# Performance work log

Hardware: AMD Instinct MI355X
Metric: run time of the kernel (lower is better)

Reference implementation:

```python
import jax, jax.numpy as jnp
import numpy as np

B, CIN, COUT, RES, WDIM, K, GN_GROUPS = 8, 512, 512, 64, 512, 3, 32


def setup_inputs() -> dict:
    key = jax.random.key(0)
    ks = jax.random.split(key, 6)
    return dict(
        x=jax.random.normal(ks[0], (B, CIN, RES, RES), jnp.float32),
        w=jax.random.normal(ks[1], (B, WDIM), jnp.float32),
        noise=jax.random.normal(ks[2], (B, 1, RES, RES), jnp.float32),
        weight=jax.random.normal(ks[3], (COUT, CIN, K, K), jnp.float32),
        bias=jnp.zeros((COUT,), jnp.float32),
        affine_W=jax.random.normal(ks[4], (3 * CIN, WDIM), jnp.float32),
        affine_b=jnp.ones((3 * CIN,), jnp.float32),  # bias_init=1
        gn_weight=jnp.ones((CIN,), jnp.float32),
        gn_bias=jnp.zeros((CIN,), jnp.float32),
        gamma=jnp.full((1, COUT, 1, 1), 1e-5, jnp.float32),  # layer_scale_init
        noise_strength=jnp.asarray(0.1, jnp.float32),
    )


def _group_norm_f32(x, weight, bias, groups=GN_GROUPS, eps=1e-5):
    # GroupNorm_float32: normalize in float32, cast back to x.dtype
    b, c, h, w = x.shape
    xf = x.astype(jnp.float32).reshape(b, groups, c // groups, h, w)
    mu = xf.mean(axis=(2, 3, 4), keepdims=True)
    var = xf.var(axis=(2, 3, 4), keepdims=True)
    xn = ((xf - mu) * jax.lax.rsqrt(var + eps)).reshape(b, c, h, w)
    return (xn * weight[None, :, None, None] + bias[None, :, None, None]).astype(x.dtype)


def reference(x, w, noise, weight, bias, affine_W, affine_b, gn_weight, gn_bias, gamma, noise_strength):
    b, cin, h, wd = x.shape
    cout, _, kh, kw = weight.shape
    # StyleSplit: FullyConnectedLayer (weight scaled by 1/sqrt(in_features)) then m1*m2+m3
    s = w @ (affine_W.T / jnp.sqrt(jnp.float32(w.shape[1]))) + affine_b  # [B, 3*Cin]
    m1, m2, m3 = jnp.split(s, 3, axis=1)
    styles = m1 * m2 + m3  # [B, Cin]
    # residual path: GroupNorm (float32) first
    xn = _group_norm_f32(x, gn_weight, gn_bias)
    # modulated_conv2d (fused path): per-sample modulate + demodulate
    wmod = weight[None] * styles[:, None, :, None, None]                 # [B,Cout,Cin,K,K]
    dcoef = jax.lax.rsqrt(jnp.sum(jnp.square(wmod), axis=(2, 3, 4)) + 1e-8)  # [B,Cout]
    wmod = wmod * dcoef[:, :, None, None, None]
    # grouped conv with groups = batch (StyleGAN batch-as-groups trick)
    xg = xn.reshape(1, b * cin, h, wd)
    wg = wmod.reshape(b * cout, cin, kh, kw)
    pad = kh // 2
    y = jax.lax.conv_general_dilated(
        xg, wg, window_strides=(1, 1), padding=[(pad, pad), (pad, pad)],
        dimension_numbers=('NCHW', 'OIHW', 'NCHW'), feature_group_count=b)
    y = y.reshape(b, cout, h, wd)
    # noise injection
    y = y + noise * noise_strength
    # fused bias + lrelu with gain = bias_def_gain['lrelu'] * gain = sqrt(2) * 2
    act_gain = np.sqrt(2.0) * 2.0
    y = jax.nn.leaky_relu(y + bias[None, :, None, None], 0.2) * act_gain
    # layer-scale + residual (residual uses the normalized x) * sqrt(2)
    y = (gamma * y + xn) * np.sqrt(2.0)
    return y
```

## Files before the change

### kernel.cpp

```cpp
#include <hip/hip_runtime.h>
#include <hip/hip_bf16.h>

typedef short short8 __attribute__((ext_vector_type(8)));
typedef float f32x4 __attribute__((ext_vector_type(4)));

#define SWZ(c) (((c) & 3) ^ (((c) >> 2) & 3))
#define UNROLL _Pragma("unroll")

static __device__ __forceinline__ unsigned short f2bf(float f) {
    union { float f; unsigned u; } v; v.f = f;
    unsigned r = v.u + 0x7FFFu + ((v.u >> 16) & 1u);
    return (unsigned short)(r >> 16);
}

static __device__ __forceinline__ void gload16(const void* g, void* l) {
    __builtin_amdgcn_global_load_lds(
        (const __attribute__((address_space(1))) unsigned int*)g,
        (__attribute__((address_space(3))) unsigned int*)l, 16, 0, 0);
}

__global__ __launch_bounds__(256) void prep1(
    const float* __restrict__ x, const float* __restrict__ w,
    const float* __restrict__ affW, const float* __restrict__ affb,
    const float* __restrict__ weight,
    float* __restrict__ styles, float* __restrict__ meanv,
    float* __restrict__ rstdv, unsigned short* __restrict__ wpk,
    unsigned short* __restrict__ zp)
{
    __shared__ float ld[9 * 128];
    __shared__ float rs[4], rq[4];
    const int bid = blockIdx.x, t = threadIdx.x;

    if (bid < 256) {
        const float4* p = (const float4*)(x + (size_t)bid * 65536);
        float s = 0.f, q = 0.f;
#pragma unroll 4
        for (int k = 0; k < 64; ++k) {
            float4 v = p[t + (k << 8)];
            s += v.x + v.y + v.z + v.w;
            q += v.x * v.x + v.y * v.y + v.z * v.z + v.w * v.w;
        }
        for (int off = 32; off; off >>= 1) { s += __shfl_xor(s, off); q += __shfl_xor(q, off); }
        if ((t & 63) == 0) { rs[t >> 6] = s; rq[t >> 6] = q; }
        __syncthreads();
        if (t == 0) {
            float S = rs[0] + rs[1] + rs[2] + rs[3];
            float Q = rq[0] + rq[1] + rq[2] + rq[3];
            float mu = S * (1.f / 65536.f);
            float var = Q * (1.f / 65536.f) - mu * mu;
            meanv[bid] = mu;
            rstdv[bid] = rsqrtf(var + 1e-5f);
        }
    } else if (bid < 512) {
        int idx = bid - 256, bx = idx & 31, b = idx >> 5;
        int lane = t & 63, wv = t >> 6;
        float wr[8];
        const float* wb = w + b * 512 + lane * 8;
        UNROLL for (int r = 0; r < 8; ++r) wr[r] = wb[r];
        for (int ii = 0; ii < 4; ++ii) {
            int i = bx * 16 + wv * 4 + ii;
            float d[3];
            UNROLL for (int jj = 0; jj < 3; ++jj) {
                const float* a = affW + (size_t)(jj * 512 + i) * 512 + lane * 8;
                float dd = 0.f;
                UNROLL for (int r = 0; r < 8; ++r) dd += wr[r] * a[r];
                for (int off = 32; off; off >>= 1) dd += __shfl_xor(dd, off);
                d[jj] = dd;
            }
            if (lane == 0) {
                const float inv = 0.044194173824159216f;
                float s0 = d[0] * inv + affb[i];
                float s1 = d[1] * inv + affb[512 + i];
                float s2 = d[2] * inv + affb[1024 + i];
                styles[b * 512 + i] = s0 * s1 + s2;
            }
        }
    } else if (bid < 2560) {
        int idx = bid - 512, co = idx >> 2, c4 = idx & 3;
        const float* src = weight + (size_t)co * 4608 + c4 * 1152;
        for (int f = t; f < 1152; f += 256)
            ld[(f % 9) * 128 + (f / 9)] = src[f];
        __syncthreads();
        unsigned short* dst = wpk + (size_t)co * 4608 + c4 * 128;
        for (int f = t; f < 1152; f += 256) {
            int tap = f >> 7, ci = f & 127;
            dst[tap * 512 + ci] = f2bf(ld[tap * 128 + ci]);
        }
    } else {
        *(short8*)&zp[t * 8] = (short8)0;
    }
}

__global__ __launch_bounds__(256) void prep2(
    const float* __restrict__ x, const float* __restrict__ weight,
    const float* __restrict__ styles, const float* __restrict__ gnw,
    const float* __restrict__ gnb, const float* __restrict__ meanv,
    const float* __restrict__ rstdv,
    float* __restrict__ dcoef, unsigned short* __restrict__ xm)
{
    __shared__ float st2[8 * 512];
    __shared__ float red[32];
    __shared__ float sA[512], sB[512];
    __shared__ unsigned short tr[32 * 520];
    const int bid = blockIdx.x, t = threadIdx.x;

    if (bid < 512) {
        int co = bid;
        for (int i = t; i < 4096; i += 256) { float s = styles[i]; st2[i] = s * s; }
        __syncthreads();
        float p[8] = {0, 0, 0, 0, 0, 0, 0, 0};
        UNROLL for (int half = 0; half < 2; ++half) {
            int ci = t * 2 + half;
            const float* wp = weight + ((size_t)co * 512 + ci) * 9;
            float wsq = 0.f;
            UNROLL for (int k = 0; k < 9; ++k) wsq += wp[k] * wp[k];
            UNROLL for (int b = 0; b < 8; ++b) p[b] += wsq * st2[b * 512 + ci];
        }
        int lane = t & 63, wv = t >> 6;
        UNROLL for (int b = 0; b < 8; ++b) {
            float v = p[b];
            for (int off = 32; off; off >>= 1) v += __shfl_xor(v, off);
            if (lane == 0) red[wv * 8 + b] = v;
        }
        __syncthreads();
        if (t < 8) {
            float s = red[t] + red[8 + t] + red[16 + t] + red[24 + t];
            dcoef[t * 512 + co] = rsqrtf(s + 1e-8f);
        }
    } else {
        int idx = bid - 512, b = idx >> 7, px0 = (idx & 127) * 32;
        for (int i = t; i < 512; i += 256) {
            int g = i >> 4;
            float mu = meanv[b * 32 + g], r = rstdv[b * 32 + g];
            float st = styles[b * 512 + i];
            float a = r * gnw[i];
            sA[i] = a * st;
            sB[i] = (gnb[i] - mu * a) * st;
        }
        __syncthreads();
        int p = t & 31, cb = t >> 5;
        const float* xb = x + (size_t)b * 512 * 4096 + px0 + p;
#pragma unroll 4
        for (int it = 0; it < 64; ++it) {
            int ci = cb + (it << 3);
            float v = xb[(size_t)ci * 4096];
            tr[p * 520 + ci] = f2bf(v * sA[ci] + sB[ci]);
        }
        __syncthreads();
        int gran = t & 63;
        UNROLL for (int k = 0; k < 8; ++k) {
            int pl = k * 4 + (t >> 6);
            short8 v = *(const short8*)&tr[pl * 520 + gran * 8];
            *(short8*)&xm[((size_t)(b * 4096 + px0 + pl) << 9) + gran * 8] = v;
        }
    }
}

#define STAGE_W(SLOT, CC_, DY_)                                                 \
    { char* wd_ = wlds + (SLOT) * 24576; int wadd_ = (DY_) * 1536 + (CC_) * 32; \
      UNROLL for (int q = 0; q < 3; ++q)                                        \
          gload16(wsrc_fix[q] + wadd_, wd_ + wdst_off[q]); }

#define STAGE_I(CC_)                                                            \
    { char* id_ = ilds + ((CC_) & 1) * 42240; int iadd_ = (CC_) * 32;           \
      UNROLL for (int q = 0; q < 5; ++q)                                        \
          gload16(isrc_fix[q] + iadd_, id_ + idst_off[q]); }

#define PHASE(DY, CCSEL, VMN, STAGES_)                                          \
  {                                                                             \
    char* wbase = wlds + (DY) * 24576;                                          \
    char* ibase = ilds + (CCSEL) * 42240 + (2 * wn + (DY)) * 4224;              \
    short8 a0[4], b0[8], a1[4], b1[8], a2[4], b2[8];                            \
    UNROLL for (int m = 0; m < 4; ++m)                                          \
        a0[m] = *(const short8*)(wbase + aoff[m]);                              \
    UNROLL for (int n = 0; n < 8; ++n)                                          \
        b0[n] = *(const short8*)(ibase + (n >> 2) * 4224 + boff[0][n & 3]);     \
    STAGES_                                                                     \
    asm volatile("s_barrier" ::: "memory");                                     \
    UNROLL for (int m = 0; m < 4; ++m)                                          \
        a1[m] = *(const short8*)(wbase + 8192 + aoff[m]);                       \
    UNROLL for (int n = 0; n < 8; ++n)                                          \
        b1[n] = *(const short8*)(ibase + (n >> 2) * 4224 + boff[1][n & 3]);     \
    __builtin_amdgcn_s_setprio(1);                                              \
    UNROLL for (int m = 0; m < 4; ++m)                                          \
        UNROLL for (int n = 0; n < 8; ++n)                                      \
            acc[m][n] = __builtin_amdgcn_mfma_f32_16x16x32_bf16(                \
                a0[m], b0[n], acc[m][n], 0, 0, 0);                              \
    UNROLL for (int m = 0; m < 4; ++m)                                          \
        a2[m] = *(const short8*)(wbase + 16384 + aoff[m]);                      \
    UNROLL for (int n = 0; n < 8; ++n)                                          \
        b2[n] = *(const short8*)(ibase + (n >> 2) * 4224 + boff[2][n & 3]);     \
    UNROLL for (int m = 0; m < 4; ++m)                                          \
        UNROLL for (int n = 0; n < 8; ++n)                                      \
            acc[m][n] = __builtin_amdgcn_mfma_f32_16x16x32_bf16(                \
                a1[m], b1[n], acc[m][n], 0, 0, 0);                              \
    UNROLL for (int m = 0; m < 4; ++m)                                          \
        UNROLL for (int n = 0; n < 8; ++n)                                      \
            acc[m][n] = __builtin_amdgcn_mfma_f32_16x16x32_bf16(                \
                a2[m], b2[n], acc[m][n], 0, 0, 0);                              \
    __builtin_amdgcn_s_setprio(0);                                              \
    asm volatile("s_waitcnt vmcnt(" #VMN ")" ::: "memory");                     \
    asm volatile("s_barrier" ::: "memory");                                     \
  }

__global__ __launch_bounds__(512, 2) void conv3(
    const unsigned short* __restrict__ xm, const unsigned short* __restrict__ wpk,
    const unsigned short* __restrict__ zp,
    const float* __restrict__ x, const float* __restrict__ noise,
    const float* __restrict__ bias, const float* __restrict__ gnw,
    const float* __restrict__ gnb, const float* __restrict__ gamma,
    const float* __restrict__ dcoef, const float* __restrict__ meanv,
    const float* __restrict__ rstdv, const float* __restrict__ nsp,
    float* __restrict__ out)
{
    extern __shared__ char smem[];
    char* wlds = smem;
    char* ilds = smem + 73728;

    const int tid = threadIdx.x, lane = tid & 63, wv = tid >> 6;
    const int ct = blockIdx.x, pt = blockIdx.y, b = blockIdx.z;
    const int co0 = ct * 128, h0 = pt * 8;
    const int wm = wv >> 2, wn = wv & 3;
    const int lm = lane & 15, lg = lane >> 4;

    if (tid < 160) {
        int sel = tid / 80, rem = tid % 80;
        int r = rem >> 3, col = ((rem >> 2) & 1) * 65, g = rem & 3;
        *(short8*)(ilds + sel * 42240 + r * 4224 + col * 64 + g * 16) = (short8)0;
    }

    const unsigned short* wsrc_fix[3]; int wdst_off[3];
    UNROLL for (int q = 0; q < 3; ++q) {
        int k = q * 8 + wv;
        int id = k * 64 + lane;
        int dxid = id >> 9, co = (id >> 2) & 127, g = (id & 3) ^ SWZ(co);
        wsrc_fix[q] = wpk + (size_t)(co0 + co) * 4608 + dxid * 512 + g * 8;
        wdst_off[q] = k * 1024;
    }
    const unsigned short* isrc_fix[5]; int idst_off[5];
    UNROLL for (int q = 0; q < 5; ++q) {
        int k = q * 8 + wv;
        int r = k >> 2, chunk = k & 3;
        int idx = chunk * 64 + lane;
        int cimg = idx >> 2, gs = (idx & 3) ^ SWZ(cimg + 1);
        int imgrow = h0 - 1 + r;
        isrc_fix[q] = ((unsigned)imgrow < 64u)
            ? xm + (((size_t)(b * 4096 + imgrow * 64 + cimg)) << 9) + gs * 8
            : zp;
        idst_off[q] = r * 4224 + 64 + chunk * 1024;
    }

    int aoff[4];
    UNROLL for (int m = 0; m < 4; ++m) {
        int col = wm * 64 + m * 16 + lm;
        aoff[m] = col * 64 + (lg ^ SWZ(col)) * 16;
    }
    int boff[3][4];
    UNROLL for (int dx = 0; dx < 3; ++dx)
        UNROLL for (int nc = 0; nc < 4; ++nc) {
            int c = nc * 16 + lm + dx;
            boff[dx][nc] = c * 64 + (lg ^ SWZ(c)) * 16;
        }

    f32x4 acc[4][8];
    UNROLL for (int m = 0; m < 4; ++m)
        UNROLL for (int n = 0; n < 8; ++n) acc[m][n] = (f32x4){0.f, 0.f, 0.f, 0.f};

    STAGE_W(0, 0, 0)
    STAGE_I(0)
    STAGE_W(1, 0, 1)
    asm volatile("s_waitcnt lgkmcnt(0)" ::: "memory");
    asm volatile("s_waitcnt vmcnt(3)" ::: "memory");
    asm volatile("s_barrier" ::: "memory");

#pragma unroll 1
    for (int cc = 0; cc < 15; ++cc) {
        const int cs = cc & 1;
        PHASE(0, cs, 8, STAGE_W(2, cc, 2) STAGE_I(cc + 1))
        PHASE(1, cs, 8, STAGE_W(0, cc + 1, 0))
        PHASE(2, cs, 3, STAGE_W(1, cc + 1, 1))
    }
    PHASE(0, 1, 3, STAGE_W(2, 15, 2))
    PHASE(1, 1, 0, {})
    PHASE(2, 1, 0, {})

    const float nsv = *nsp;
    UNROLL for (int m = 0; m < 4; ++m) {
        UNROLL for (int n = 0; n < 8; ++n) {
            int pix = (h0 + 2 * wn + (n >> 2)) * 64 + (n & 3) * 16 + lm;
            float nz = noise[b * 4096 + pix] * nsv;
            UNROLL for (int j = 0; j < 4; ++j) {
                int co = co0 + wm * 64 + m * 16 + lg * 4 + j;
                int gidx = co >> 4;
                float v = acc[m][n][j] * dcoef[b * 512 + co] + nz + bias[co];
                float act = (v > 0.f ? v : 0.2f * v) * 2.8284271247461903f;
                float xv = x[((size_t)(b * 512 + co)) * 4096 + pix];
                float xn = (xv - meanv[b * 32 + gidx]) * rstdv[b * 32 + gidx] * gnw[co] + gnb[co];
                out[((size_t)(b * 512 + co)) * 4096 + pix] =
                    (gamma[co] * act + xn) * 1.4142135623730951f;
            }
        }
    }
}

extern "C" void kernel_launch(void* const* d_in, const int* in_sizes, int n_in,
                              void* d_out, int out_size, void* d_ws, size_t ws_size,
                              hipStream_t stream) {
    const float* x      = (const float*)d_in[0];
    const float* w      = (const float*)d_in[1];
    const float* noise  = (const float*)d_in[2];
    const float* weight = (const float*)d_in[3];
    const float* bias   = (const float*)d_in[4];
    const float* affW   = (const float*)d_in[5];
    const float* affb   = (const float*)d_in[6];
    const float* gnw    = (const float*)d_in[7];
    const float* gnb    = (const float*)d_in[8];
    const float* gamma  = (const float*)d_in[9];
    const float* nsp    = (const float*)d_in[10];
    float* out = (float*)d_out;

    char* ws = (char*)d_ws;
    float* styles = (float*)(ws + 0);
    float* dcoef  = (float*)(ws + 16384);
    float* meanv  = (float*)(ws + 32768);
    float* rstdv  = (float*)(ws + 33792);
    unsigned short* zp  = (unsigned short*)(ws + 34816);
    unsigned short* wpk = (unsigned short*)(ws + 38912);
    unsigned short* xm  = (unsigned short*)(ws + 4757504);

    hipFuncSetAttribute(reinterpret_cast<const void*>(conv3),
                        hipFuncAttributeMaxDynamicSharedMemorySize, 158208);

    prep1<<<dim3(2561), 256, 0, stream>>>(x, w, affW, affb, weight,
                                          styles, meanv, rstdv, wpk, zp);
    prep2<<<dim3(1536), 256, 0, stream>>>(x, weight, styles, gnw, gnb,
                                          meanv, rstdv, dcoef, xm);
    conv3<<<dim3(4, 8, 8), 512, 158208, stream>>>(xm, wpk, zp, x, noise, bias, gnw, gnb,
                                                  gamma, dcoef, meanv, rstdv, nsp, out);
}
```

Before: 302.4 us.

## Load conv weights directly from global into registers using 32x32 MFMA

Weights are repacked into an MFMA-fragment-friendly layout so each wave reads its A operands straight from global memory into registers. This removes the LDS weight staging and frees LDS, and the inner loop switches from 16x16x32 to 32x32x16 bf16 MFMA with a one-tap register prefetch. The epilogue also hoists the per-channel constants. In exchange, weight loads now go through global/L2 with no reuse across waves, so global load latency may be exposed.

```diff
diff --git a/kernel.cpp b/kernel.cpp
--- a/kernel.cpp
+++ b/kernel.cpp
@@ -2,7 +2,7 @@
 #include <hip/hip_bf16.h>
 
 typedef short short8 __attribute__((ext_vector_type(8)));
-typedef float f32x4 __attribute__((ext_vector_type(4)));
+typedef float f32x16 __attribute__((ext_vector_type(16)));
 
 #define SWZ(c) (((c) & 3) ^ (((c) >> 2) & 3))
 #define UNROLL _Pragma("unroll")
@@ -24,10 +24,10 @@
     const float* __restrict__ affW, const float* __restrict__ affb,
     const float* __restrict__ weight,
     float* __restrict__ styles, float* __restrict__ meanv,
-    float* __restrict__ rstdv, unsigned short* __restrict__ wpk,
+    float* __restrict__ rstdv, unsigned short* __restrict__ wpk2,
     unsigned short* __restrict__ zp)
 {
-    __shared__ float ld[9 * 128];
+    __shared__ float ld[4608];
     __shared__ float rs[4], rq[4];
     const int bid = blockIdx.x, t = threadIdx.x;
 
@@ -75,16 +75,17 @@
                 styles[b * 512 + i] = s0 * s1 + s2;
             }
         }
-    } else if (bid < 2560) {
-        int idx = bid - 512, co = idx >> 2, c4 = idx & 3;
-        const float* src = weight + (size_t)co * 4608 + c4 * 1152;
-        for (int f = t; f < 1152; f += 256)
-            ld[(f % 9) * 128 + (f / 9)] = src[f];
-        __syncthreads();
-        unsigned short* dst = wpk + (size_t)co * 4608 + c4 * 128;
-        for (int f = t; f < 1152; f += 256) {
-            int tap = f >> 7, ci = f & 127;
-            dst[tap * 512 + ci] = f2bf(ld[tap * 128 + ci]);
+    } else if (bid < 1024) {
+        int co = bid - 512;
+        const float* src = weight + (size_t)co * 4608;
+        for (int f = t; f < 4608; f += 256)
+            ld[(f % 9) * 512 + (f / 9)] = src[f];
+        __syncthreads();
+        for (int idx = t; idx < 4608; idx += 256) {
+            int tap = idx >> 9, ci = idx & 511;
+            int kk = ci >> 4, c16 = ci & 15;
+            wpk2[((size_t)(tap * 32 + kk) * 512 + co) * 16 + c16] =
+                f2bf(ld[tap * 512 + ci]);
         }
     } else {
         *(short8*)&zp[t * 8] = (short8)0;
@@ -156,55 +157,13 @@
     }
 }
 
-#define STAGE_W(SLOT, CC_, DY_)                                                 \
-    { char* wd_ = wlds + (SLOT) * 24576; int wadd_ = (DY_) * 1536 + (CC_) * 32; \
-      UNROLL for (int q = 0; q < 3; ++q)                                        \
-          gload16(wsrc_fix[q] + wadd_, wd_ + wdst_off[q]); }
-
 #define STAGE_I(CC_)                                                            \
     { char* id_ = ilds + ((CC_) & 1) * 42240; int iadd_ = (CC_) * 32;           \
       UNROLL for (int q = 0; q < 5; ++q)                                        \
           gload16(isrc_fix[q] + iadd_, id_ + idst_off[q]); }
 
-#define PHASE(DY, CCSEL, VMN, STAGES_)                                          \
-  {                                                                             \
-    char* wbase = wlds + (DY) * 24576;                                          \
-    char* ibase = ilds + (CCSEL) * 42240 + (2 * wn + (DY)) * 4224;              \
-    short8 a0[4], b0[8], a1[4], b1[8], a2[4], b2[8];                            \
-    UNROLL for (int m = 0; m < 4; ++m)                                          \
-        a0[m] = *(const short8*)(wbase + aoff[m]);                              \
-    UNROLL for (int n = 0; n < 8; ++n)                                          \
-        b0[n] = *(const short8*)(ibase + (n >> 2) * 4224 + boff[0][n & 3]);     \
-    STAGES_                                                                     \
-    asm volatile("s_barrier" ::: "memory");                                     \
-    UNROLL for (int m = 0; m < 4; ++m)                                          \
-        a1[m] = *(const short8*)(wbase + 8192 + aoff[m]);                       \
-    UNROLL for (int n = 0; n < 8; ++n)                                          \
-        b1[n] = *(const short8*)(ibase + (n >> 2) * 4224 + boff[1][n & 3]);     \
-    __builtin_amdgcn_s_setprio(1);                                              \
-    UNROLL for (int m = 0; m < 4; ++m)                                          \
-        UNROLL for (int n = 0; n < 8; ++n)                                      \
-            acc[m][n] = __builtin_amdgcn_mfma_f32_16x16x32_bf16(                \
-                a0[m], b0[n], acc[m][n], 0, 0, 0);                              \
-    UNROLL for (int m = 0; m < 4; ++m)                                          \
-        a2[m] = *(const short8*)(wbase + 16384 + aoff[m]);                      \
-    UNROLL for (int n = 0; n < 8; ++n)                                          \
-        b2[n] = *(const short8*)(ibase + (n >> 2) * 4224 + boff[2][n & 3]);     \
-    UNROLL for (int m = 0; m < 4; ++m)                                          \
-        UNROLL for (int n = 0; n < 8; ++n)                                      \
-            acc[m][n] = __builtin_amdgcn_mfma_f32_16x16x32_bf16(                \
-                a1[m], b1[n], acc[m][n], 0, 0, 0);                              \
-    UNROLL for (int m = 0; m < 4; ++m)                                          \
-        UNROLL for (int n = 0; n < 8; ++n)                                      \
-            acc[m][n] = __builtin_amdgcn_mfma_f32_16x16x32_bf16(                \
-                a2[m], b2[n], acc[m][n], 0, 0, 0);                              \
-    __builtin_amdgcn_s_setprio(0);                                              \
-    asm volatile("s_waitcnt vmcnt(" #VMN ")" ::: "memory");                     \
-    asm volatile("s_barrier" ::: "memory");                                     \
-  }
-
 __global__ __launch_bounds__(512, 2) void conv3(
-    const unsigned short* __restrict__ xm, const unsigned short* __restrict__ wpk,
+    const unsigned short* __restrict__ xm, const unsigned short* __restrict__ wpk2,
     const unsigned short* __restrict__ zp,
     const float* __restrict__ x, const float* __restrict__ noise,
     const float* __restrict__ bias, const float* __restrict__ gnw,
@@ -213,15 +172,12 @@
     const float* __restrict__ rstdv, const float* __restrict__ nsp,
     float* __restrict__ out)
 {
-    extern __shared__ char smem[];
-    char* wlds = smem;
-    char* ilds = smem + 73728;
+    extern __shared__ char ilds[];
 
     const int tid = threadIdx.x, lane = tid & 63, wv = tid >> 6;
     const int ct = blockIdx.x, pt = blockIdx.y, b = blockIdx.z;
     const int co0 = ct * 128, h0 = pt * 8;
     const int wm = wv >> 2, wn = wv & 3;
-    const int lm = lane & 15, lg = lane >> 4;
 
     if (tid < 160) {
         int sel = tid / 80, rem = tid % 80;
@@ -229,14 +185,6 @@
         *(short8*)(ilds + sel * 42240 + r * 4224 + col * 64 + g * 16) = (short8)0;
     }
 
-    const unsigned short* wsrc_fix[3]; int wdst_off[3];
-    UNROLL for (int q = 0; q < 3; ++q) {
-        int k = q * 8 + wv;
-        int id = k * 64 + lane;
-        int dxid = id >> 9, co = (id >> 2) & 127, g = (id & 3) ^ SWZ(co);
-        wsrc_fix[q] = wpk + (size_t)(co0 + co) * 4608 + dxid * 512 + g * 8;
-        wdst_off[q] = k * 1024;
-    }
     const unsigned short* isrc_fix[5]; int idst_off[5];
     UNROLL for (int q = 0; q < 5; ++q) {
         int k = q * 8 + wv;
@@ -250,54 +198,83 @@
         idst_off[q] = r * 4224 + 64 + chunk * 1024;
     }
 
-    int aoff[4];
-    UNROLL for (int m = 0; m < 4; ++m) {
-        int col = wm * 64 + m * 16 + lm;
-        aoff[m] = col * 64 + (lg ^ SWZ(col)) * 16;
-    }
-    int boff[3][4];
-    UNROLL for (int dx = 0; dx < 3; ++dx)
-        UNROLL for (int nc = 0; nc < 4; ++nc) {
-            int c = nc * 16 + lm + dx;
-            boff[dx][nc] = c * 64 + (lg ^ SWZ(c)) * 16;
-        }
-
-    f32x4 acc[4][8];
-    UNROLL for (int m = 0; m < 4; ++m)
-        UNROLL for (int n = 0; n < 8; ++n) acc[m][n] = (f32x4){0.f, 0.f, 0.f, 0.f};
-
-    STAGE_W(0, 0, 0)
+    const unsigned short* wA = wpk2
+        + (size_t)(co0 + wm * 64 + (lane & 31)) * 16 + (lane >> 5) * 8;
+
+    int bo[2][3][2];
+    UNROLL for (int ch = 0; ch < 2; ++ch)
+        UNROLL for (int dx = 0; dx < 3; ++dx) {
+            int c = ch * 32 + (lane & 31) + dx;
+            UNROLL for (int s = 0; s < 2; ++s)
+                bo[ch][dx][s] = c * 64 + (((s * 2 + (lane >> 5)) ^ SWZ(c)) * 16);
+        }
+
+    f32x16 acc[2][4];
+    UNROLL for (int m = 0; m < 2; ++m)
+        UNROLL for (int n = 0; n < 4; ++n) acc[m][n] = (f32x16)(0.0f);
+
     STAGE_I(0)
-    STAGE_W(1, 0, 1)
-    asm volatile("s_waitcnt lgkmcnt(0)" ::: "memory");
-    asm volatile("s_waitcnt vmcnt(3)" ::: "memory");
+    short8 a0q[4];
+    UNROLL for (int m = 0; m < 2; ++m)
+        UNROLL for (int s = 0; s < 2; ++s)
+            a0q[m * 2 + s] = *(const short8*)(wA + s * 8192 + m * 512);
+    asm volatile("s_waitcnt vmcnt(0) lgkmcnt(0)" ::: "memory");
     asm volatile("s_barrier" ::: "memory");
 
 #pragma unroll 1
-    for (int cc = 0; cc < 15; ++cc) {
-        const int cs = cc & 1;
-        PHASE(0, cs, 8, STAGE_W(2, cc, 2) STAGE_I(cc + 1))
-        PHASE(1, cs, 8, STAGE_W(0, cc + 1, 0))
-        PHASE(2, cs, 3, STAGE_W(1, cc + 1, 1))
-    }
-    PHASE(0, 1, 3, STAGE_W(2, 15, 2))
-    PHASE(1, 1, 0, {})
-    PHASE(2, 1, 0, {})
+    for (int cc = 0; cc < 16; ++cc) {
+        if (cc < 15) STAGE_I(cc + 1)
+        const unsigned short* wAc = wA + cc * 16384;
+        const unsigned short* wAn = wA + (cc < 15 ? cc + 1 : 15) * 16384;
+        char* ib = ilds + (cc & 1) * 42240;
+        UNROLL for (int t = 0; t < 9; ++t) {
+            const int dy = t / 3, dx = t % 3;
+            const unsigned short* wT =
+                (t < 8) ? (wAc + (size_t)(t + 1) * 262144) : wAn;
+            short8 a1q[4];
+            UNROLL for (int m = 0; m < 2; ++m)
+                UNROLL for (int s = 0; s < 2; ++s)
+                    a1q[m * 2 + s] = *(const short8*)(wT + s * 8192 + m * 512);
+            char* r0 = ib + (2 * wn + dy) * 4224;
+            short8 bv[8];
+            UNROLL for (int nt = 0; nt < 4; ++nt)
+                UNROLL for (int s = 0; s < 2; ++s)
+                    bv[nt * 2 + s] = *(const short8*)
+                        (r0 + (nt >> 1) * 4224 + bo[nt & 1][dx][s]);
+            __builtin_amdgcn_s_setprio(1);
+            UNROLL for (int s = 0; s < 2; ++s)
+                UNROLL for (int m = 0; m < 2; ++m)
+                    UNROLL for (int nt = 0; nt < 4; ++nt)
+                        acc[m][nt] = __builtin_amdgcn_mfma_f32_32x32x16_bf16(
+                            a0q[m * 2 + s], bv[nt * 2 + s], acc[m][nt], 0, 0, 0);
+            __builtin_amdgcn_s_setprio(0);
+            UNROLL for (int q = 0; q < 4; ++q) a0q[q] = a1q[q];
+        }
+        asm volatile("s_waitcnt vmcnt(4)" ::: "memory");
+        asm volatile("s_barrier" ::: "memory");
+    }
 
     const float nsv = *nsp;
-    UNROLL for (int m = 0; m < 4; ++m) {
-        UNROLL for (int n = 0; n < 8; ++n) {
-            int pix = (h0 + 2 * wn + (n >> 2)) * 64 + (n & 3) * 16 + lm;
-            float nz = noise[b * 4096 + pix] * nsv;
-            UNROLL for (int j = 0; j < 4; ++j) {
-                int co = co0 + wm * 64 + m * 16 + lg * 4 + j;
-                int gidx = co >> 4;
-                float v = acc[m][n][j] * dcoef[b * 512 + co] + nz + bias[co];
+    const int lg2 = lane >> 5;
+    float nzv[4]; int pixv[4];
+    UNROLL for (int nt = 0; nt < 4; ++nt) {
+        pixv[nt] = (h0 + 2 * wn + (nt >> 1)) * 64 + (nt & 1) * 32 + (lane & 31);
+        nzv[nt] = noise[b * 4096 + pixv[nt]] * nsv;
+    }
+    UNROLL for (int m = 0; m < 2; ++m) {
+        UNROLL for (int r = 0; r < 16; ++r) {
+            int co = co0 + wm * 64 + m * 32 + (r & 3) + 8 * (r >> 2) + 4 * lg2;
+            int gidx = co >> 4;
+            float dc = dcoef[b * 512 + co], bs = bias[co], gm = gamma[co];
+            float a = rstdv[b * 32 + gidx] * gnw[co];
+            float bsh = gnb[co] - meanv[b * 32 + gidx] * a;
+            const float* xrow = x + ((size_t)(b * 512 + co)) * 4096;
+            float* orow = out + ((size_t)(b * 512 + co)) * 4096;
+            UNROLL for (int nt = 0; nt < 4; ++nt) {
+                float v = acc[m][nt][r] * dc + nzv[nt] + bs;
                 float act = (v > 0.f ? v : 0.2f * v) * 2.8284271247461903f;
-                float xv = x[((size_t)(b * 512 + co)) * 4096 + pix];
-                float xn = (xv - meanv[b * 32 + gidx]) * rstdv[b * 32 + gidx] * gnw[co] + gnb[co];
-                out[((size_t)(b * 512 + co)) * 4096 + pix] =
-                    (gamma[co] * act + xn) * 1.4142135623730951f;
+                float xn = xrow[pixv[nt]] * a + bsh;
+                orow[pixv[nt]] = (gm * act + xn) * 1.4142135623730951f;
             }
         }
     }
@@ -324,17 +301,18 @@
     float* dcoef  = (float*)(ws + 16384);
     float* meanv  = (float*)(ws + 32768);
     float* rstdv  = (float*)(ws + 33792);
-    unsigned short* zp  = (unsigned short*)(ws + 34816);
-    unsigned short* wpk = (unsigned short*)(ws + 38912);
-    unsigned short* xm  = (unsigned short*)(ws + 4757504);
+    unsigned short* zp   = (unsigned short*)(ws + 34816);
+    unsigned short* wpk2 = (unsigned short*)(ws + 38912);
+    unsigned short* xm   = (unsigned short*)(ws + 4757504);
 
     hipFuncSetAttribute(reinterpret_cast<const void*>(conv3),
-                        hipFuncAttributeMaxDynamicSharedMemorySize, 158208);
-
-    prep1<<<dim3(2561), 256, 0, stream>>>(x, w, affW, affb, weight,
-                                          styles, meanv, rstdv, wpk, zp);
+                        hipFuncAttributeMaxDynamicSharedMemorySize, 84480);
+
+    prep1<<<dim3(1025), 256, 0, stream>>>(x, w, affW, affb, weight,
+                                          styles, meanv, rstdv, wpk2, zp);
     prep2<<<dim3(1536), 256, 0, stream>>>(x, weight, styles, gnw, gnb,
                                           meanv, rstdv, dcoef, xm);
-    conv3<<<dim3(4, 8, 8), 512, 158208, stream>>>(xm, wpk, zp, x, noise, bias, gnw, gnb,
-                                                  gamma, dcoef, meanv, rstdv, nsp, out);
-}
+    conv3<<<dim3(4, 8, 8), 512, 84480, stream>>>(xm, wpk2, zp, x, noise, bias,
+                                                 gnw, gnb, gamma, dcoef,
+                                                 meanv, rstdv, nsp, out);
+}
```

New measurement: 299.2 us. Within noise of the previous version (-1.1%).
